# Kernel tuning notes

Measured on AMD Instinct MI355X. Metric: run time of the kernel, lower is better.

The kernel has to match this reference:

```python
import jax, jax.numpy as jnp
import numpy as np

D_MODEL = 2048
HIDDEN = int(2 * D_MODEL * 4 / 3)  # 5461


def ternary_quant(w):
    # BitNet b1.58-style per-tensor ternary quantization with STE.
    s = jnp.mean(jnp.abs(w))
    q = jnp.clip(jnp.round(w / s), -1.0, 1.0) * s
    return w + jax.lax.stop_gradient(q - w)


def setup_inputs() -> dict:
    key = jax.random.key(0)
    k0, k1, k2, k3 = jax.random.split(key, 4)
    x = jax.random.normal(k0, (4, 4096, D_MODEL), dtype=jnp.float32)
    # torch nn.Linear weights are [out_features, in_features]
    std_in = 1.0 / np.sqrt(D_MODEL)
    std_h = 1.0 / np.sqrt(HIDDEN)
    w1 = jax.random.uniform(k1, (HIDDEN, D_MODEL), jnp.float32, -std_in, std_in)
    w3 = jax.random.uniform(k2, (HIDDEN, D_MODEL), jnp.float32, -std_in, std_in)
    w2 = jax.random.uniform(k3, (D_MODEL, HIDDEN), jnp.float32, -std_h, std_h)
    return {"x": x, "w1": w1, "w3": w3, "w2": w2}


def reference(x, w1, w3, w2):
    w1q = ternary_quant(w1)
    w3q = ternary_quant(w3)
    w2q = ternary_quant(w2)
    h1 = jnp.einsum("bsd,hd->bsh", x, w1q)  # [B,S,H]
    h3 = jnp.einsum("bsd,hd->bsh", x, w3q)  # [B,S,H]
    g = jax.nn.silu(h1) * h3
    return jnp.einsum("bsh,dh->bsd", g, w2q)  # [B,S,D]
```

## Files before the change

### kernel.cpp

```cpp
#include <hip/hip_runtime.h>
#include <cmath>

typedef unsigned short u16;
typedef unsigned char u8;
typedef unsigned int u32;
typedef float f32x4 __attribute__((ext_vector_type(4)));
typedef int i32x4 __attribute__((ext_vector_type(4)));
typedef short s16x8 __attribute__((ext_vector_type(8)));
typedef u32 u32x4 __attribute__((ext_vector_type(4)));

#define D_MODEL 2048
#define HIDDEN  5461
#define HPAD    5504
#define WCNT    11184128
#define XSCALE  4096.0f

__device__ __forceinline__ u16 f2bf(float f) {
  union { float f; u32 u; } c; c.f = f;
  u32 u = c.u + 0x7fffu + ((c.u >> 16) & 1u);
  return (u16)(u >> 16);
}

__device__ __forceinline__ void async16(const void* g, void* l) {
  __builtin_amdgcn_global_load_lds(
      (const __attribute__((address_space(1))) unsigned int*)g,
      (__attribute__((address_space(3))) unsigned int*)l, 16, 0, 0);
}

__global__ void zero_sums_kernel(double* __restrict__ s) {
  if (threadIdx.x < 3) s[threadIdx.x] = 0.0;
}

__global__ void abssum_kernel(const float* __restrict__ w, long n, double* __restrict__ out) {
  long i0 = ((long)blockIdx.x * blockDim.x + threadIdx.x) * 4;
  long stride = (long)gridDim.x * blockDim.x * 4;
  double s = 0.0;
  for (long i = i0; i < n; i += stride) {
    float4 v = *(const float4*)(w + i);
    s += (double)fabsf(v.x) + (double)fabsf(v.y) + (double)fabsf(v.z) + (double)fabsf(v.w);
  }
#pragma unroll
  for (int off = 32; off > 0; off >>= 1) s += __shfl_down(s, off, 64);
  __shared__ double ls[4];
  int lane = threadIdx.x & 63, wv = threadIdx.x >> 6;
  if (lane == 0) ls[wv] = s;
  __syncthreads();
  if (threadIdx.x == 0) atomicAdd(out, ls[0] + ls[1] + ls[2] + ls[3]);
}

__global__ void quant13_kernel(const float* __restrict__ w, const double* __restrict__ sum,
                               char* __restrict__ ws) {
  double s = *sum * (1.0 / (double)WCNT);
  int nt = blockIdx.x;
  int c  = blockIdx.y * 256 + threadIdx.x;
  int col = c & 63;
  int kg  = c >> 6;
  int n = nt * 64 + col;
  u32x4 qv = {0u, 0u, 0u, 0u};
  if (n < HIDDEN) {
    const float* row = w + (long)n * D_MODEL + kg * 16;
#pragma unroll
    for (int q4 = 0; q4 < 4; ++q4) {
      float4 v = *(const float4*)(row + q4 * 4);
      float vv[4] = {v.x, v.y, v.z, v.w};
      u32 word = 0;
#pragma unroll
      for (int e = 0; e < 4; ++e) {
        int qi = (int)fmin(fmax(rint((double)vv[e] / s), -1.0), 1.0);
        word |= ((u32)(u8)(char)qi) << (8 * e);
      }
      qv[q4] = word;
    }
  }
  *(u32x4*)(ws + (long)nt * 131072 + ((long)kg * 64 + col) * 16) = qv;
}

__global__ void quant2_kernel(const float* __restrict__ w, const double* __restrict__ sum,
                              u16* __restrict__ ws) {
  double s = *sum * (1.0 / (double)WCNT);
  int nt = blockIdx.x;
  int kc = blockIdx.y;
  int nn = threadIdx.x & 127;
  int kl = threadIdx.x >> 7;
  int n = nt * 128 + nn;
  long base = (long)nt * 704512;
#pragma unroll
  for (int it = 0; it < 4; ++it) {
    int kgl = kl + it * 2;
    int kg = kc * 8 + kgl;
    s16x8 qv;
#pragma unroll
    for (int j = 0; j < 8; ++j) {
      int k = kg * 8 + j;
      float q = 0.f;
      if (k < HIDDEN) {
        float v = w[(long)n * HIDDEN + k];
        q = (float)fmin(fmax(rint((double)v / s), -1.0), 1.0);
      }
      qv[j] = (short)f2bf(q);
    }
    *(s16x8*)(ws + base + ((long)kg * 128 + nn) * 8) = qv;
  }
}

__global__ void xquant_kernel(const float* __restrict__ x, u8* __restrict__ xhi,
                              u8* __restrict__ xlo) {
  int mt = blockIdx.x;
  int c  = blockIdx.y * 256 + threadIdx.x;
  int row = c & 127;
  int kg  = c >> 7;
  const float* src = x + ((long)mt * 128 + row) * D_MODEL + kg * 16;
  u32x4 hv, lv;
#pragma unroll
  for (int q4 = 0; q4 < 4; ++q4) {
    float4 v = *(const float4*)(src + q4 * 4);
    float vv[4] = {v.x, v.y, v.z, v.w};
    u32 hw = 0, lw = 0;
#pragma unroll
    for (int e = 0; e < 4; ++e) {
      float f = fminf(fmaxf(vv[e] * XSCALE, -32639.f), 32639.f);
      int tt = (int)rintf(f) + 128;
      hw |= ((u32)((tt >> 8) & 0xFF)) << (8 * e);
      lw |= ((u32)((tt ^ 0x80) & 0xFF)) << (8 * e);
    }
    hv[q4] = hw; lv[q4] = lw;
  }
  long o = (long)mt * 262144 + ((long)kg * 128 + row) * 16;
  *(u32x4*)(xhi + o) = hv;
  *(u32x4*)(xlo + o) = lv;
}

__global__ __launch_bounds__(256, 2)
void gemm1_kernel(const u8* __restrict__ xhi, const u8* __restrict__ xlo,
                  const char* __restrict__ w1s, const char* __restrict__ w3s,
                  const double* __restrict__ sums, u16* __restrict__ gs, int mt0) {
  __shared__ alignas(16) u8 Ahi[8192];
  __shared__ alignas(16) u8 Alo[8192];
  __shared__ alignas(16) u8 B1s[4096];
  __shared__ alignas(16) u8 B3s[4096];
  const int mtl = blockIdx.x;
  const int nt  = blockIdx.y;
  const int mtg = mt0 + mtl;
  const int t = threadIdx.x;
  const int lane = t & 63, wave = t >> 6;
  const int wm = wave >> 1, wn = wave & 1;
  const int quad = lane >> 4;
  const int rowA = wm * 64 + (lane & 15);
  const int rowB = wn * 32 + (lane & 15);

  i32x4 a1h[4][2], a1l[4][2], a3h[4][2], a3l[4][2];
#pragma unroll
  for (int i = 0; i < 4; ++i)
#pragma unroll
    for (int j = 0; j < 2; ++j) {
      a1h[i][j] = {0, 0, 0, 0}; a1l[i][j] = {0, 0, 0, 0};
      a3h[i][j] = {0, 0, 0, 0}; a3l[i][j] = {0, 0, 0, 0};
    }

  const u8* Ah = xhi + (long)mtg * 262144 + t * 16;
  const u8* Al = xlo + (long)mtg * 262144 + t * 16;
  const char* B1 = w1s + (long)nt * 131072 + t * 16;
  const char* B3 = w3s + (long)nt * 131072 + t * 16;

  for (int c = 0; c < 32; ++c) {
    async16(Ah + c * 8192,        &Ahi[t * 16]);
    async16(Ah + c * 8192 + 4096, &Ahi[4096 + t * 16]);
    async16(Al + c * 8192,        &Alo[t * 16]);
    async16(Al + c * 8192 + 4096, &Alo[4096 + t * 16]);
    async16(B1 + c * 4096, &B1s[t * 16]);
    async16(B3 + c * 4096, &B3s[t * 16]);
    __syncthreads();
    i32x4 b1f[2], b3f[2], ah[4], al[4];
#pragma unroll
    for (int j = 0; j < 2; ++j) {
      b1f[j] = *(const i32x4*)&B1s[quad * 1024 + (rowB + j * 16) * 16];
      b3f[j] = *(const i32x4*)&B3s[quad * 1024 + (rowB + j * 16) * 16];
    }
#pragma unroll
    for (int i = 0; i < 4; ++i) {
      ah[i] = *(const i32x4*)&Ahi[quad * 2048 + (rowA + i * 16) * 16];
      al[i] = *(const i32x4*)&Alo[quad * 2048 + (rowA + i * 16) * 16];
    }
#pragma unroll
    for (int i = 0; i < 4; ++i)
#pragma unroll
      for (int j = 0; j < 2; ++j) {
        a1h[i][j] = __builtin_amdgcn_mfma_i32_16x16x64_i8(ah[i], b1f[j], a1h[i][j], 0, 0, 0);
        a1l[i][j] = __builtin_amdgcn_mfma_i32_16x16x64_i8(al[i], b1f[j], a1l[i][j], 0, 0, 0);
        a3h[i][j] = __builtin_amdgcn_mfma_i32_16x16x64_i8(ah[i], b3f[j], a3h[i][j], 0, 0, 0);
        a3l[i][j] = __builtin_amdgcn_mfma_i32_16x16x64_i8(al[i], b3f[j], a3l[i][j], 0, 0, 0);
      }
    __syncthreads();
  }

  const float sc1 = (float)(sums[0] * (1.0 / (double)WCNT)) / XSCALE;
  const float sc3 = (float)(sums[1] * (1.0 / (double)WCNT)) / XSCALE;
  u16* gb = gs + (long)mtl * 704512;
#pragma unroll
  for (int i = 0; i < 4; ++i) {
#pragma unroll
    for (int j = 0; j < 2; ++j) {
      const int h = nt * 64 + wn * 32 + j * 16 + (lane & 15);
      const int kg2 = h >> 3, jj = h & 7;
#pragma unroll
      for (int rr = 0; rr < 4; ++rr) {
        const int mm = wm * 64 + i * 16 + quad * 4 + rr;
        float h1 = (float)(a1h[i][j][rr] * 256 + a1l[i][j][rr]) * sc1;
        float h3 = (float)(a3h[i][j][rr] * 256 + a3l[i][j][rr]) * sc3;
        float g = (h1 / (1.0f + expf(-h1))) * h3;
        gb[((long)kg2 * 128 + mm) * 8 + jj] = f2bf(g);
      }
    }
  }
}

__global__ __launch_bounds__(256, 2)
void gemm2_kernel(const u16* __restrict__ gs, const u16* __restrict__ w2s,
                  const double* __restrict__ sums, float* __restrict__ out) {
  __shared__ alignas(16) u16 As[8192];
  __shared__ alignas(16) u16 Bs[8192];
  const int mt = blockIdx.x, nt = blockIdx.y;
  const int t = threadIdx.x;
  const int lane = t & 63, wave = t >> 6;
  const int wm = wave >> 1, wn = wave & 1;
  const int quad = lane >> 4;
  const int rowA = wm * 64 + (lane & 15);
  const int rowB = wn * 64 + (lane & 15);

  f32x4 acc[4][4];
#pragma unroll
  for (int i = 0; i < 4; ++i)
#pragma unroll
    for (int j = 0; j < 4; ++j) acc[i][j] = {0.f, 0.f, 0.f, 0.f};

  const u16* Ab = gs  + (long)mt * 704512 + t * 8;
  const u16* Bb = w2s + (long)nt * 704512 + t * 8;

  for (int c = 0; c < 86; ++c) {
    const u16* ag = Ab + (long)c * 8192;
    const u16* bg = Bb + (long)c * 8192;
#pragma unroll
    for (int j = 0; j < 4; ++j) {
      async16(ag + j * 2048, &As[t * 8 + j * 2048]);
      async16(bg + j * 2048, &Bs[t * 8 + j * 2048]);
    }
    __syncthreads();
#pragma unroll
    for (int ks = 0; ks < 2; ++ks) {
      const int kg = ks * 4 + quad;
      s16x8 af[4], bf[4];
#pragma unroll
      for (int i = 0; i < 4; ++i)
        af[i] = *(const s16x8*)&As[kg * 1024 + (rowA + i * 16) * 8];
#pragma unroll
      for (int j = 0; j < 4; ++j)
        bf[j] = *(const s16x8*)&Bs[kg * 1024 + (rowB + j * 16) * 8];
#pragma unroll
      for (int i = 0; i < 4; ++i)
#pragma unroll
        for (int j = 0; j < 4; ++j)
          acc[i][j] = __builtin_amdgcn_mfma_f32_16x16x32_bf16(af[i], bf[j], acc[i][j], 0, 0, 0);
    }
    __syncthreads();
  }

  const float s2 = (float)(sums[2] * (1.0 / (double)WCNT));
#pragma unroll
  for (int i = 0; i < 4; ++i) {
    const int r0 = wm * 64 + i * 16 + quad * 4;
#pragma unroll
    for (int j = 0; j < 4; ++j) {
      const int d = nt * 128 + wn * 64 + j * 16 + (lane & 15);
#pragma unroll
      for (int rr = 0; rr < 4; ++rr) {
        const long m = (long)mt * 128 + r0 + rr;
        out[m * D_MODEL + d] = acc[i][j][rr] * s2;
      }
    }
  }
}

extern "C" void kernel_launch(void* const* d_in, const int* in_sizes, int n_in,
                              void* d_out, int out_size, void* d_ws, size_t ws_size,
                              hipStream_t stream) {
  (void)in_sizes; (void)n_in; (void)out_size; (void)ws_size;
  const float* x  = (const float*)d_in[0];
  const float* w1 = (const float*)d_in[1];
  const float* w3 = (const float*)d_in[2];
  const float* w2 = (const float*)d_in[3];
  float* out = (float*)d_out;

  char* ws = (char*)d_ws;
  double* sums = (double*)ws;
  char* w1s = ws + 256;
  char* w3s = w1s + 11272192L;
  u16*  w2s = (u16*)(w3s + 11272192L);
  u8*   xhi = (u8*)(w3s + 11272192L + 22544384L);
  u8*   xlo = xhi + 33554432L;
  u16*  gs  = (u16*)(xlo + 33554432L);

  zero_sums_kernel<<<1, 64, 0, stream>>>(sums);
  abssum_kernel<<<1024, 256, 0, stream>>>(w1, (long)WCNT, sums + 0);
  abssum_kernel<<<1024, 256, 0, stream>>>(w3, (long)WCNT, sums + 1);
  abssum_kernel<<<1024, 256, 0, stream>>>(w2, (long)WCNT, sums + 2);

  quant13_kernel<<<dim3(86, 32), 256, 0, stream>>>(w1, sums + 0, w1s);
  quant13_kernel<<<dim3(86, 32), 256, 0, stream>>>(w3, sums + 1, w3s);
  quant2_kernel<<<dim3(16, 86), 256, 0, stream>>>(w2, sums + 2, w2s);
  xquant_kernel<<<dim3(128, 64), 256, 0, stream>>>(x, xhi, xlo);

  for (int pass = 0; pass < 2; ++pass) {
    gemm1_kernel<<<dim3(64, 86), 256, 0, stream>>>(xhi, xlo, w1s, w3s, sums, gs, pass * 64);
    gemm2_kernel<<<dim3(64, 16), 256, 0, stream>>>(gs, w2s, sums,
                                                   out + (long)pass * 64 * 128 * D_MODEL);
  }
}
```

Measured before the change: 1.473 ms.

## Triple-buffer LDS with async prefetch in both GEMM kernels

Both GEMM kernels now use a three-stage LDS ring. The next K-chunk is issued with async global-to-LDS loads before computing on the current one, and a partial vmcnt wait plus a single barrier per iteration replaces the two syncthreads. This is meant to overlap global memory latency with MFMA work. gemm2 halves its K-chunk to fit three buffers, and s_setprio is raised around the MFMA bursts. The single-barrier scheme relies on the third buffer to avoid write-after-read hazards. More LDS per block (72KB for gemm1) may limit occupancy.

```diff
diff --git a/kernel.cpp b/kernel.cpp
--- a/kernel.cpp
+++ b/kernel.cpp
@@ -134,10 +134,7 @@
 void gemm1_kernel(const u8* __restrict__ xhi, const u8* __restrict__ xlo,
                   const char* __restrict__ w1s, const char* __restrict__ w3s,
                   const double* __restrict__ sums, u16* __restrict__ gs, int mt0) {
-  __shared__ alignas(16) u8 Ahi[8192];
-  __shared__ alignas(16) u8 Alo[8192];
-  __shared__ alignas(16) u8 B1s[4096];
-  __shared__ alignas(16) u8 B3s[4096];
+  __shared__ alignas(16) u8 L[3 * 24576];
   const int mtl = blockIdx.x;
   const int nt  = blockIdx.y;
   const int mtg = mt0 + mtl;
@@ -162,25 +159,40 @@
   const char* B1 = w1s + (long)nt * 131072 + t * 16;
   const char* B3 = w3s + (long)nt * 131072 + t * 16;
 
+#define STAGE1(buf, c) do {                                      \
+    u8* Lb_ = L + (buf) * 24576;                                 \
+    async16(Ah + (c) * 8192,        Lb_ + t * 16);               \
+    async16(Ah + (c) * 8192 + 4096, Lb_ + 4096 + t * 16);        \
+    async16(Al + (c) * 8192,        Lb_ + 8192 + t * 16);        \
+    async16(Al + (c) * 8192 + 4096, Lb_ + 12288 + t * 16);       \
+    async16(B1 + (c) * 4096,        Lb_ + 16384 + t * 16);       \
+    async16(B3 + (c) * 4096,        Lb_ + 20480 + t * 16);       \
+  } while (0)
+
+  STAGE1(0, 0);
+  int cur = 0;
   for (int c = 0; c < 32; ++c) {
-    async16(Ah + c * 8192,        &Ahi[t * 16]);
-    async16(Ah + c * 8192 + 4096, &Ahi[4096 + t * 16]);
-    async16(Al + c * 8192,        &Alo[t * 16]);
-    async16(Al + c * 8192 + 4096, &Alo[4096 + t * 16]);
-    async16(B1 + c * 4096, &B1s[t * 16]);
-    async16(B3 + c * 4096, &B3s[t * 16]);
-    __syncthreads();
+    int nb = cur + 1; if (nb == 3) nb = 0;
+    if (c < 31) {
+      STAGE1(nb, c + 1);
+      asm volatile("s_waitcnt vmcnt(6)" ::: "memory");
+    } else {
+      asm volatile("s_waitcnt vmcnt(0)" ::: "memory");
+    }
+    __builtin_amdgcn_s_barrier();
+    const u8* Lb = L + cur * 24576;
     i32x4 b1f[2], b3f[2], ah[4], al[4];
 #pragma unroll
     for (int j = 0; j < 2; ++j) {
-      b1f[j] = *(const i32x4*)&B1s[quad * 1024 + (rowB + j * 16) * 16];
-      b3f[j] = *(const i32x4*)&B3s[quad * 1024 + (rowB + j * 16) * 16];
+      b1f[j] = *(const i32x4*)&Lb[16384 + quad * 1024 + (rowB + j * 16) * 16];
+      b3f[j] = *(const i32x4*)&Lb[20480 + quad * 1024 + (rowB + j * 16) * 16];
     }
 #pragma unroll
     for (int i = 0; i < 4; ++i) {
-      ah[i] = *(const i32x4*)&Ahi[quad * 2048 + (rowA + i * 16) * 16];
-      al[i] = *(const i32x4*)&Alo[quad * 2048 + (rowA + i * 16) * 16];
-    }
+      ah[i] = *(const i32x4*)&Lb[quad * 2048 + (rowA + i * 16) * 16];
+      al[i] = *(const i32x4*)&Lb[8192 + quad * 2048 + (rowA + i * 16) * 16];
+    }
+    __builtin_amdgcn_s_setprio(1);
 #pragma unroll
     for (int i = 0; i < 4; ++i)
 #pragma unroll
@@ -190,8 +202,10 @@
         a3h[i][j] = __builtin_amdgcn_mfma_i32_16x16x64_i8(ah[i], b3f[j], a3h[i][j], 0, 0, 0);
         a3l[i][j] = __builtin_amdgcn_mfma_i32_16x16x64_i8(al[i], b3f[j], a3l[i][j], 0, 0, 0);
       }
-    __syncthreads();
-  }
+    __builtin_amdgcn_s_setprio(0);
+    cur = nb;
+  }
+#undef STAGE1
 
   const float sc1 = (float)(sums[0] * (1.0 / (double)WCNT)) / XSCALE;
   const float sc3 = (float)(sums[1] * (1.0 / (double)WCNT)) / XSCALE;
@@ -217,8 +231,7 @@
 __global__ __launch_bounds__(256, 2)
 void gemm2_kernel(const u16* __restrict__ gs, const u16* __restrict__ w2s,
                   const double* __restrict__ sums, float* __restrict__ out) {
-  __shared__ alignas(16) u16 As[8192];
-  __shared__ alignas(16) u16 Bs[8192];
+  __shared__ alignas(16) u16 L[3 * 8192];
   const int mt = blockIdx.x, nt = blockIdx.y;
   const int t = threadIdx.x;
   const int lane = t & 63, wave = t >> 6;
@@ -236,33 +249,43 @@
   const u16* Ab = gs  + (long)mt * 704512 + t * 8;
   const u16* Bb = w2s + (long)nt * 704512 + t * 8;
 
-  for (int c = 0; c < 86; ++c) {
-    const u16* ag = Ab + (long)c * 8192;
-    const u16* bg = Bb + (long)c * 8192;
-#pragma unroll
-    for (int j = 0; j < 4; ++j) {
-      async16(ag + j * 2048, &As[t * 8 + j * 2048]);
-      async16(bg + j * 2048, &Bs[t * 8 + j * 2048]);
-    }
-    __syncthreads();
-#pragma unroll
-    for (int ks = 0; ks < 2; ++ks) {
-      const int kg = ks * 4 + quad;
-      s16x8 af[4], bf[4];
-#pragma unroll
-      for (int i = 0; i < 4; ++i)
-        af[i] = *(const s16x8*)&As[kg * 1024 + (rowA + i * 16) * 8];
+#define STAGE2(buf, c) do {                                      \
+    u16* Lb_ = L + (buf) * 8192;                                 \
+    async16(Ab + (c) * 4096,        Lb_ + t * 8);                \
+    async16(Ab + (c) * 4096 + 2048, Lb_ + 2048 + t * 8);         \
+    async16(Bb + (c) * 4096,        Lb_ + 4096 + t * 8);         \
+    async16(Bb + (c) * 4096 + 2048, Lb_ + 6144 + t * 8);         \
+  } while (0)
+
+  STAGE2(0, 0);
+  int cur = 0;
+  for (int c = 0; c < 172; ++c) {
+    int nb = cur + 1; if (nb == 3) nb = 0;
+    if (c < 171) {
+      STAGE2(nb, c + 1);
+      asm volatile("s_waitcnt vmcnt(4)" ::: "memory");
+    } else {
+      asm volatile("s_waitcnt vmcnt(0)" ::: "memory");
+    }
+    __builtin_amdgcn_s_barrier();
+    const u16* Lb = L + cur * 8192;
+    s16x8 af[4], bf[4];
+#pragma unroll
+    for (int i = 0; i < 4; ++i)
+      af[i] = *(const s16x8*)&Lb[quad * 1024 + (rowA + i * 16) * 8];
+#pragma unroll
+    for (int j = 0; j < 4; ++j)
+      bf[j] = *(const s16x8*)&Lb[4096 + quad * 1024 + (rowB + j * 16) * 8];
+    __builtin_amdgcn_s_setprio(1);
+#pragma unroll
+    for (int i = 0; i < 4; ++i)
 #pragma unroll
       for (int j = 0; j < 4; ++j)
-        bf[j] = *(const s16x8*)&Bs[kg * 1024 + (rowB + j * 16) * 8];
-#pragma unroll
-      for (int i = 0; i < 4; ++i)
-#pragma unroll
-        for (int j = 0; j < 4; ++j)
-          acc[i][j] = __builtin_amdgcn_mfma_f32_16x16x32_bf16(af[i], bf[j], acc[i][j], 0, 0, 0);
-    }
-    __syncthreads();
-  }
+        acc[i][j] = __builtin_amdgcn_mfma_f32_16x16x32_bf16(af[i], bf[j], acc[i][j], 0, 0, 0);
+    __builtin_amdgcn_s_setprio(0);
+    cur = nb;
+  }
+#undef STAGE2
 
   const float s2 = (float)(sums[2] * (1.0 / (double)WCNT));
 #pragma unroll
```

Result: faster. 1.345 ms (-8.7%).
